# Optimization experiments

Hardware: AMD Instinct MI355X
Metric: run time of the kernel (lower is better)

## Reference

```python
import jax, jax.numpy as jnp
import numpy as np

N_ATOMS = 262144
N_SEG = 2048
DIM = 256
OUT_DIM = 256


def setup_inputs() -> dict:
    key = jax.random.key(0)
    k1, k2, k3, k4 = jax.random.split(key, 4)
    atom_features = jax.random.normal(k1, (N_ATOMS, DIM), dtype=jnp.float32)
    # ragged segment offsets: 0 = off[0] < off[1] < ... < off[S] = N_ATOMS
    rng = np.random.default_rng(0)
    interior = np.sort(rng.choice(np.arange(1, N_ATOMS), size=N_SEG - 1, replace=False))
    index_list = jnp.asarray(np.concatenate([[0], interior, [N_ATOMS]]), dtype=jnp.int64)
    # SelfAttentionPooling params: attention scorer + output projection
    Wa = jax.random.normal(k2, (DIM, 1), dtype=jnp.float32) / np.sqrt(DIM)
    ba = jnp.zeros((1,), dtype=jnp.float32)
    Wo = jax.random.normal(k3, (DIM, OUT_DIM), dtype=jnp.float32) / np.sqrt(DIM)
    bo = jnp.zeros((OUT_DIM,), dtype=jnp.float32)
    return {"atom_features": atom_features, "index_list": index_list,
            "Wa": Wa, "ba": ba, "Wo": Wo, "bo": bo}


def reference(atom_features, index_list, Wa, ba, Wo, bo):
    S = index_list.shape[0] - 1          # number of segments (static)
    N = atom_features.shape[0]
    # segment id of each atom from the offsets vector
    seg = jnp.searchsorted(index_list, jnp.arange(N), side="right") - 1  # [N]
    # per-atom attention logits
    logits = (atom_features @ Wa + ba)[:, 0]                             # [N]
    # segment-wise stable softmax
    seg_max = jax.ops.segment_max(logits, seg, num_segments=S)           # [S]
    e = jnp.exp(logits - seg_max[seg])                                   # [N]
    denom = jax.ops.segment_sum(e, seg, num_segments=S)                  # [S]
    att = e / denom[seg]                                                 # [N]
    # attention-weighted pooling per segment
    pooled = jax.ops.segment_sum(att[:, None] * atom_features, seg, num_segments=S)  # [S, DIM]
    return pooled @ Wo + bo                                              # [S, OUT_DIM]
```

## Files before the change

### kernel.cpp

```cpp
#include <hip/hip_runtime.h>

#define DIM 256
#define NSEG 2048
#define NATOMS 262144
#define TA 8
#define NTILES (NATOMS / TA)
#define SLOTS (NSEG + NTILES)

__device__ __forceinline__ long long load_off(const void* p, int i, int is64) {
  if (is64) return ((const long long*)p)[i];
  return (long long)((const int*)p)[i];
}

__global__ void seg_of_tile(const void* __restrict__ offs_raw,
                            int* __restrict__ s0tab)
{
  int s = blockIdx.x * blockDim.x + threadIdx.x;
  if (s >= NSEG) return;
  const int is64 = (((const int*)offs_raw)[1] == 0);
  int lo = (int)load_off(offs_raw, s, is64);
  int hi = (int)load_off(offs_raw, s + 1, is64);
  int u0 = (lo + TA - 1) / TA;
  int u1 = (hi + TA - 1) / TA - 1;
  for (int u = u0; u <= u1; ++u) s0tab[u] = s;
  if (s == NSEG - 1) s0tab[NTILES] = NSEG - 1;
}

__global__ __launch_bounds__(256, 4)
void pool_waves(const float* __restrict__ feat,
                const void* __restrict__ offs_raw,
                const float* __restrict__ Wa,
                const int* __restrict__ s0tab,
                float* __restrict__ md,
                float* __restrict__ accbuf)
{
  const int lane = threadIdx.x & 63;
  const int wv   = threadIdx.x >> 6;
  const int u    = blockIdx.x * 4 + wv;
  const int base = u * TA;
  const int is64 = (((const int*)offs_raw)[1] == 0);

  const float4 wa4 = ((const float4*)Wa)[lane];
  const float4* fg = (const float4*)feat + (size_t)base * (DIM / 4);

  float4 r[TA];
#pragma unroll
  for (int k = 0; k < TA; ++k) r[k] = fg[(size_t)k * 64 + lane];

  const int s0  = s0tab[u];
  const int s1n = s0tab[u + 1];
  const int e1  = (int)load_off(offs_raw, s1n, is64);
  const int s1  = s1n - (e1 == base + TA ? 1 : 0);

  float lg[TA];
#pragma unroll
  for (int k = 0; k < TA; ++k) {
    float p = r[k].x * wa4.x + r[k].y * wa4.y + r[k].z * wa4.z + r[k].w * wa4.w;
    p += __shfl_xor(p, 32);
    p += __shfl_xor(p, 16);
    p += __shfl_xor(p, 8);
    p += __shfl_xor(p, 4);
    p += __shfl_xor(p, 2);
    p += __shfl_xor(p, 1);
    lg[k] = p;
  }

  if (s0 == s1) {
    float m = lg[0];
#pragma unroll
    for (int k = 1; k < TA; ++k) m = fmaxf(m, lg[k]);
    float d = 0.f;
    float4 acc = make_float4(0.f, 0.f, 0.f, 0.f);
#pragma unroll
    for (int k = 0; k < TA; ++k) {
      float e = __expf(lg[k] - m);
      d += e;
      acc.x = fmaf(e, r[k].x, acc.x);
      acc.y = fmaf(e, r[k].y, acc.y);
      acc.z = fmaf(e, r[k].z, acc.z);
      acc.w = fmaf(e, r[k].w, acc.w);
    }
    const int slot = s0 + u;
    ((float4*)(accbuf + (size_t)slot * DIM))[lane] = acc;
    if (lane == 0) { md[2 * slot] = m; md[2 * slot + 1] = d; }
  } else {
    for (int s = s0; s <= s1; ++s) {
      int lo = (int)load_off(offs_raw, s, is64);
      int hi = (int)load_off(offs_raw, s + 1, is64);
      int la = lo - base; la = la > 0 ? la : 0;
      int lb = hi - base; lb = lb < TA ? lb : TA;
      float m = -INFINITY;
#pragma unroll
      for (int k = 0; k < TA; ++k)
        if (k >= la && k < lb) m = fmaxf(m, lg[k]);
      float d = 0.f;
      float4 acc = make_float4(0.f, 0.f, 0.f, 0.f);
#pragma unroll
      for (int k = 0; k < TA; ++k) {
        bool v = (k >= la && k < lb);
        float e = v ? __expf(lg[k] - m) : 0.f;
        d += e;
        acc.x = fmaf(e, r[k].x, acc.x);
        acc.y = fmaf(e, r[k].y, acc.y);
        acc.z = fmaf(e, r[k].z, acc.z);
        acc.w = fmaf(e, r[k].w, acc.w);
      }
      const int slot = s + u;
      ((float4*)(accbuf + (size_t)slot * DIM))[lane] = acc;
      if (lane == 0) { md[2 * slot] = m; md[2 * slot + 1] = d; }
    }
  }
}

__global__ __launch_bounds__(256, 2)
void merge_project(const float* __restrict__ md,
                   const float* __restrict__ accbuf,
                   const void* __restrict__ offs_raw,
                   const float* __restrict__ Wo,
                   const float* __restrict__ bo,
                   float* __restrict__ out)
{
  __shared__ float pooled[4][DIM];
  __shared__ float sc_s[4][64];
  const int tid  = threadIdx.x;
  const int lane = tid & 63;
  const int wv   = tid >> 6;
  const int is64 = (((const int*)offs_raw)[1] == 0);
  const int s    = blockIdx.x * 4 + wv;

  {
    const int lo = (int)load_off(offs_raw, s, is64);
    const int hi = (int)load_off(offs_raw, s + 1, is64);
    const int u0 = lo / TA;
    const int u1 = (hi - 1) / TA;
    const int n  = u1 - u0 + 1;

    float M = -INFINITY, D = 0.f;
    float4 acc = make_float4(0.f, 0.f, 0.f, 0.f);

    for (int c0 = 0; c0 < n; c0 += 64) {
      const int j = c0 + lane;
      const bool v = (j < n);
      const int slot = s + u0 + j;
      float mj = v ? md[2 * slot] : -INFINITY;
      float dj = v ? md[2 * slot + 1] : 0.f;

      float Mc = mj;
      Mc = fmaxf(Mc, __shfl_xor(Mc, 32));
      Mc = fmaxf(Mc, __shfl_xor(Mc, 16));
      Mc = fmaxf(Mc, __shfl_xor(Mc, 8));
      Mc = fmaxf(Mc, __shfl_xor(Mc, 4));
      Mc = fmaxf(Mc, __shfl_xor(Mc, 2));
      Mc = fmaxf(Mc, __shfl_xor(Mc, 1));
      const float Mn = fmaxf(M, Mc);
      const float rs = (c0 == 0) ? 0.f : __expf(M - Mn);
      const float scj = __expf(mj - Mn);

      float t = dj * scj;
      t += __shfl_xor(t, 32);
      t += __shfl_xor(t, 16);
      t += __shfl_xor(t, 8);
      t += __shfl_xor(t, 4);
      t += __shfl_xor(t, 2);
      t += __shfl_xor(t, 1);
      D = D * rs + t;

      sc_s[wv][lane] = scj;

      acc.x *= rs; acc.y *= rs; acc.z *= rs; acc.w *= rs;

      const int cn = (n - c0) < 64 ? (n - c0) : 64;
      const float4* ab = (const float4*)(accbuf + (size_t)(s + u0 + c0) * DIM);
      int jj = 0;
      for (; jj + 4 <= cn; jj += 4) {
        float4 a0 = ab[(size_t)(jj + 0) * 64 + lane];
        float4 a1 = ab[(size_t)(jj + 1) * 64 + lane];
        float4 a2 = ab[(size_t)(jj + 2) * 64 + lane];
        float4 a3 = ab[(size_t)(jj + 3) * 64 + lane];
        float s0 = sc_s[wv][jj + 0], s1 = sc_s[wv][jj + 1];
        float s2 = sc_s[wv][jj + 2], s3 = sc_s[wv][jj + 3];
        acc.x = fmaf(s0, a0.x, fmaf(s1, a1.x, fmaf(s2, a2.x, fmaf(s3, a3.x, acc.x))));
        acc.y = fmaf(s0, a0.y, fmaf(s1, a1.y, fmaf(s2, a2.y, fmaf(s3, a3.y, acc.y))));
        acc.z = fmaf(s0, a0.z, fmaf(s1, a1.z, fmaf(s2, a2.z, fmaf(s3, a3.z, acc.z))));
        acc.w = fmaf(s0, a0.w, fmaf(s1, a1.w, fmaf(s2, a2.w, fmaf(s3, a3.w, acc.w))));
      }
      for (; jj < cn; ++jj) {
        float4 a0 = ab[(size_t)jj * 64 + lane];
        float s0 = sc_s[wv][jj];
        acc.x = fmaf(s0, a0.x, acc.x);
        acc.y = fmaf(s0, a0.y, acc.y);
        acc.z = fmaf(s0, a0.z, acc.z);
        acc.w = fmaf(s0, a0.w, acc.w);
      }
      M = Mn;
    }

    const float inv = 1.f / D;
    ((float4*)pooled[wv])[lane] =
        make_float4(acc.x * inv, acc.y * inv, acc.z * inv, acc.w * inv);
  }
  __syncthreads();

  float o0 = 0.f, o1 = 0.f, o2 = 0.f, o3 = 0.f;
  for (int k = 0; k < DIM; ++k) {
    float w = Wo[k * DIM + tid];
    o0 = fmaf(pooled[0][k], w, o0);
    o1 = fmaf(pooled[1][k], w, o1);
    o2 = fmaf(pooled[2][k], w, o2);
    o3 = fmaf(pooled[3][k], w, o3);
  }
  const float b = bo[tid];
  const int sb = blockIdx.x * 4;
  out[(size_t)(sb + 0) * DIM + tid] = o0 + b;
  out[(size_t)(sb + 1) * DIM + tid] = o1 + b;
  out[(size_t)(sb + 2) * DIM + tid] = o2 + b;
  out[(size_t)(sb + 3) * DIM + tid] = o3 + b;
}

extern "C" void kernel_launch(void* const* d_in, const int* in_sizes, int n_in,
                              void* d_out, int out_size, void* d_ws, size_t ws_size,
                              hipStream_t stream)
{
  const float* feat = (const float*)d_in[0];
  const void*  offs = d_in[1];
  const float* Wa   = (const float*)d_in[2];
  const float* Wo   = (const float*)d_in[4];
  const float* bo   = (const float*)d_in[5];
  float* out = (float*)d_out;

  float* md     = (float*)d_ws;
  float* accbuf = md + 2 * SLOTS;
  int*   s0tab  = (int*)(accbuf + (size_t)SLOTS * DIM);

  hipLaunchKernelGGL(seg_of_tile, dim3((NSEG + 255) / 256), dim3(256), 0, stream,
                     offs, s0tab);
  hipLaunchKernelGGL(pool_waves, dim3(NTILES / 4), dim3(256), 0, stream,
                     feat, offs, Wa, s0tab, md, accbuf);
  hipLaunchKernelGGL(merge_project, dim3(NSEG / 4), dim3(256), 0, stream,
                     md, accbuf, offs, Wo, bo, out);
}
```

Before: 79.86 us.

## Process four tiles per wave with double-buffered loads and DPP reductions

Each wave now handles four 8-atom tiles instead of one. Loads of the next tile are issued before the current tile is processed, using two register buffers, so memory latency overlaps with compute. The cross-lane logit reduction switches from shuffles to DPP and swizzle intrinsics. A precomputed s1tab replaces the extra offset lookup that found each tile's last segment. The cost is more registers per wave and a grid four times smaller, which may lower occupancy.

```diff
diff --git a/kernel.cpp b/kernel.cpp
--- a/kernel.cpp
+++ b/kernel.cpp
@@ -6,110 +6,143 @@
 #define TA 8
 #define NTILES (NATOMS / TA)
 #define SLOTS (NSEG + NTILES)
+#define TPW 4
+#define WPB 4
+#define NBLK (NTILES / (WPB * TPW))
 
 __device__ __forceinline__ long long load_off(const void* p, int i, int is64) {
   if (is64) return ((const long long*)p)[i];
   return (long long)((const int*)p)[i];
 }
 
+__device__ __forceinline__ float wave_sum_b(float v) {
+  int x;
+  x = __builtin_amdgcn_update_dpp(0, __float_as_int(v), 0xB1, 0xF, 0xF, true);
+  v += __int_as_float(x);
+  x = __builtin_amdgcn_update_dpp(0, __float_as_int(v), 0x4E, 0xF, 0xF, true);
+  v += __int_as_float(x);
+  x = __builtin_amdgcn_update_dpp(0, __float_as_int(v), 0x141, 0xF, 0xF, true);
+  v += __int_as_float(x);
+  x = __builtin_amdgcn_update_dpp(0, __float_as_int(v), 0x140, 0xF, 0xF, true);
+  v += __int_as_float(x);
+  v += __int_as_float(__builtin_amdgcn_ds_swizzle(__float_as_int(v), 0x401F));
+  v += __shfl_xor(v, 32);
+  return v;
+}
+
 __global__ void seg_of_tile(const void* __restrict__ offs_raw,
-                            int* __restrict__ s0tab)
+                            int* __restrict__ s0tab,
+                            int* __restrict__ s1tab)
 {
   int s = blockIdx.x * blockDim.x + threadIdx.x;
   if (s >= NSEG) return;
   const int is64 = (((const int*)offs_raw)[1] == 0);
-  int lo = (int)load_off(offs_raw, s, is64);
-  int hi = (int)load_off(offs_raw, s + 1, is64);
-  int u0 = (lo + TA - 1) / TA;
-  int u1 = (hi + TA - 1) / TA - 1;
-  for (int u = u0; u <= u1; ++u) s0tab[u] = s;
-  if (s == NSEG - 1) s0tab[NTILES] = NSEG - 1;
-}
+  const int lo = (int)load_off(offs_raw, s, is64);
+  const int hi = (int)load_off(offs_raw, s + 1, is64);
+  {
+    int u0 = (lo + TA - 1) / TA;
+    int u1 = (hi + TA - 1) / TA - 1;
+    for (int u = u0; u <= u1; ++u) s0tab[u] = s;
+  }
+  {
+    int u0 = lo / TA;
+    int u1 = hi >= TA ? (hi - TA) / TA : -1;
+    for (int u = u0; u <= u1; ++u) s1tab[u] = s;
+  }
+}
+
+#define LOADT(R, sA, sB, uu) do {                                         \
+    const float4* fg_ = (const float4*)feat + (size_t)(uu) * (TA * 64);   \
+    _Pragma("unroll")                                                     \
+    for (int k_ = 0; k_ < TA; ++k_) R[k_] = fg_[k_ * 64 + lane];          \
+    sA = s0tab[(uu)];                                                     \
+    sB = s1tab[(uu)];                                                     \
+  } while (0)
+
+#define PROCT(R, sA, sB, uu) do {                                         \
+    const int base_ = (uu) * TA;                                          \
+    float lg_[TA];                                                        \
+    _Pragma("unroll")                                                     \
+    for (int k_ = 0; k_ < TA; ++k_) {                                     \
+      float p_ = R[k_].x * wa4.x + R[k_].y * wa4.y +                      \
+                 R[k_].z * wa4.z + R[k_].w * wa4.w;                       \
+      lg_[k_] = wave_sum_b(p_);                                           \
+    }                                                                     \
+    if (sA == sB) {                                                       \
+      float m_ = lg_[0];                                                  \
+      _Pragma("unroll")                                                   \
+      for (int k_ = 1; k_ < TA; ++k_) m_ = fmaxf(m_, lg_[k_]);            \
+      float d_ = 0.f;                                                     \
+      float4 acc_ = make_float4(0.f, 0.f, 0.f, 0.f);                      \
+      _Pragma("unroll")                                                   \
+      for (int k_ = 0; k_ < TA; ++k_) {                                   \
+        float e_ = __expf(lg_[k_] - m_);                                  \
+        d_ += e_;                                                         \
+        acc_.x = fmaf(e_, R[k_].x, acc_.x);                               \
+        acc_.y = fmaf(e_, R[k_].y, acc_.y);                               \
+        acc_.z = fmaf(e_, R[k_].z, acc_.z);                               \
+        acc_.w = fmaf(e_, R[k_].w, acc_.w);                               \
+      }                                                                   \
+      const int slot_ = sA + (uu);                                        \
+      ((float4*)(accbuf + (size_t)slot_ * DIM))[lane] = acc_;             \
+      if (lane == 0) { md[2 * slot_] = m_; md[2 * slot_ + 1] = d_; }      \
+    } else {                                                              \
+      for (int s_ = sA; s_ <= sB; ++s_) {                                 \
+        int lo_ = (int)load_off(offs_raw, s_, is64);                      \
+        int hi_ = (int)load_off(offs_raw, s_ + 1, is64);                  \
+        int la_ = lo_ - base_; la_ = la_ > 0 ? la_ : 0;                   \
+        int lb_ = hi_ - base_; lb_ = lb_ < TA ? lb_ : TA;                 \
+        float m_ = -INFINITY;                                             \
+        _Pragma("unroll")                                                 \
+        for (int k_ = 0; k_ < TA; ++k_)                                   \
+          if (k_ >= la_ && k_ < lb_) m_ = fmaxf(m_, lg_[k_]);             \
+        float d_ = 0.f;                                                   \
+        float4 acc_ = make_float4(0.f, 0.f, 0.f, 0.f);                    \
+        _Pragma("unroll")                                                 \
+        for (int k_ = 0; k_ < TA; ++k_) {                                 \
+          bool v_ = (k_ >= la_ && k_ < lb_);                              \
+          float e_ = v_ ? __expf(lg_[k_] - m_) : 0.f;                     \
+          d_ += e_;                                                       \
+          acc_.x = fmaf(e_, R[k_].x, acc_.x);                             \
+          acc_.y = fmaf(e_, R[k_].y, acc_.y);                             \
+          acc_.z = fmaf(e_, R[k_].z, acc_.z);                             \
+          acc_.w = fmaf(e_, R[k_].w, acc_.w);                             \
+        }                                                                 \
+        const int slot_ = s_ + (uu);                                      \
+        ((float4*)(accbuf + (size_t)slot_ * DIM))[lane] = acc_;           \
+        if (lane == 0) { md[2 * slot_] = m_; md[2 * slot_ + 1] = d_; }    \
+      }                                                                   \
+    }                                                                     \
+  } while (0)
 
 __global__ __launch_bounds__(256, 4)
 void pool_waves(const float* __restrict__ feat,
                 const void* __restrict__ offs_raw,
                 const float* __restrict__ Wa,
                 const int* __restrict__ s0tab,
+                const int* __restrict__ s1tab,
                 float* __restrict__ md,
                 float* __restrict__ accbuf)
 {
   const int lane = threadIdx.x & 63;
   const int wv   = threadIdx.x >> 6;
-  const int u    = blockIdx.x * 4 + wv;
-  const int base = u * TA;
+  const int wid  = blockIdx.x * WPB + wv;
+  const int u0   = wid * TPW;
   const int is64 = (((const int*)offs_raw)[1] == 0);
 
   const float4 wa4 = ((const float4*)Wa)[lane];
-  const float4* fg = (const float4*)feat + (size_t)base * (DIM / 4);
-
-  float4 r[TA];
-#pragma unroll
-  for (int k = 0; k < TA; ++k) r[k] = fg[(size_t)k * 64 + lane];
-
-  const int s0  = s0tab[u];
-  const int s1n = s0tab[u + 1];
-  const int e1  = (int)load_off(offs_raw, s1n, is64);
-  const int s1  = s1n - (e1 == base + TA ? 1 : 0);
-
-  float lg[TA];
-#pragma unroll
-  for (int k = 0; k < TA; ++k) {
-    float p = r[k].x * wa4.x + r[k].y * wa4.y + r[k].z * wa4.z + r[k].w * wa4.w;
-    p += __shfl_xor(p, 32);
-    p += __shfl_xor(p, 16);
-    p += __shfl_xor(p, 8);
-    p += __shfl_xor(p, 4);
-    p += __shfl_xor(p, 2);
-    p += __shfl_xor(p, 1);
-    lg[k] = p;
-  }
-
-  if (s0 == s1) {
-    float m = lg[0];
-#pragma unroll
-    for (int k = 1; k < TA; ++k) m = fmaxf(m, lg[k]);
-    float d = 0.f;
-    float4 acc = make_float4(0.f, 0.f, 0.f, 0.f);
-#pragma unroll
-    for (int k = 0; k < TA; ++k) {
-      float e = __expf(lg[k] - m);
-      d += e;
-      acc.x = fmaf(e, r[k].x, acc.x);
-      acc.y = fmaf(e, r[k].y, acc.y);
-      acc.z = fmaf(e, r[k].z, acc.z);
-      acc.w = fmaf(e, r[k].w, acc.w);
-    }
-    const int slot = s0 + u;
-    ((float4*)(accbuf + (size_t)slot * DIM))[lane] = acc;
-    if (lane == 0) { md[2 * slot] = m; md[2 * slot + 1] = d; }
-  } else {
-    for (int s = s0; s <= s1; ++s) {
-      int lo = (int)load_off(offs_raw, s, is64);
-      int hi = (int)load_off(offs_raw, s + 1, is64);
-      int la = lo - base; la = la > 0 ? la : 0;
-      int lb = hi - base; lb = lb < TA ? lb : TA;
-      float m = -INFINITY;
-#pragma unroll
-      for (int k = 0; k < TA; ++k)
-        if (k >= la && k < lb) m = fmaxf(m, lg[k]);
-      float d = 0.f;
-      float4 acc = make_float4(0.f, 0.f, 0.f, 0.f);
-#pragma unroll
-      for (int k = 0; k < TA; ++k) {
-        bool v = (k >= la && k < lb);
-        float e = v ? __expf(lg[k] - m) : 0.f;
-        d += e;
-        acc.x = fmaf(e, r[k].x, acc.x);
-        acc.y = fmaf(e, r[k].y, acc.y);
-        acc.z = fmaf(e, r[k].z, acc.z);
-        acc.w = fmaf(e, r[k].w, acc.w);
-      }
-      const int slot = s + u;
-      ((float4*)(accbuf + (size_t)slot * DIM))[lane] = acc;
-      if (lane == 0) { md[2 * slot] = m; md[2 * slot + 1] = d; }
-    }
-  }
+
+  float4 A[TA], B[TA];
+  int sA0, sB0, sA1, sB1;
+
+  LOADT(A, sA0, sB0, u0 + 0);
+  LOADT(B, sA1, sB1, u0 + 1);
+  PROCT(A, sA0, sB0, u0 + 0);
+  LOADT(A, sA0, sB0, u0 + 2);
+  PROCT(B, sA1, sB1, u0 + 1);
+  LOADT(B, sA1, sB1, u0 + 3);
+  PROCT(A, sA0, sB0, u0 + 2);
+  PROCT(B, sA1, sB1, u0 + 3);
 }
 
 __global__ __launch_bounds__(256, 2)
@@ -231,11 +264,12 @@
   float* md     = (float*)d_ws;
   float* accbuf = md + 2 * SLOTS;
   int*   s0tab  = (int*)(accbuf + (size_t)SLOTS * DIM);
+  int*   s1tab  = s0tab + NTILES;
 
   hipLaunchKernelGGL(seg_of_tile, dim3((NSEG + 255) / 256), dim3(256), 0, stream,
-                     offs, s0tab);
-  hipLaunchKernelGGL(pool_waves, dim3(NTILES / 4), dim3(256), 0, stream,
-                     feat, offs, Wa, s0tab, md, accbuf);
+                     offs, s0tab, s1tab);
+  hipLaunchKernelGGL(pool_waves, dim3(NBLK), dim3(256), 0, stream,
+                     feat, offs, Wa, s0tab, s1tab, md, accbuf);
   hipLaunchKernelGGL(merge_project, dim3(NSEG / 4), dim3(256), 0, stream,
                      md, accbuf, offs, Wo, bo, out);
 }
```

After: 84.25 us. 1.06x slower.
